# Kernel tuning notes

Measured on AMD Instinct MI355X. Metric: run time of the kernel, lower is better.

Reference implementation:

```python
import math
import jax, jax.numpy as jnp
import numpy as np

N_HEADS = 12
D_EMBED = 768
BATCH = 2
SEQ = 2048


def setup_inputs() -> dict:
    key = jax.random.key(0)
    ks = jax.random.split(key, 5)
    scale = 0.02
    return {
        "x": jax.random.normal(ks[0], (BATCH, SEQ, D_EMBED), dtype=jnp.float32),
        "w_in": jax.random.normal(ks[1], (D_EMBED, 3 * D_EMBED), dtype=jnp.float32) * scale,
        "b_in": jax.random.normal(ks[2], (3 * D_EMBED,), dtype=jnp.float32) * scale,
        "w_out": jax.random.normal(ks[3], (D_EMBED, D_EMBED), dtype=jnp.float32) * scale,
        "b_out": jax.random.normal(ks[4], (D_EMBED,), dtype=jnp.float32) * scale,
    }


def reference(x, w_in, b_in, w_out, b_out):
    # x: [B, S, D]
    B, S, D = x.shape
    H = N_HEADS
    dh = D // H
    # Fused QKV projection: [B, S, 3D]
    qkv = x @ w_in + b_in
    q, k, v = jnp.split(qkv, 3, axis=-1)
    # [B, S, D] -> [B, H, S, dh]
    def to_heads(t):
        return t.reshape(B, S, H, dh).transpose(0, 2, 1, 3)
    q, k, v = to_heads(q), to_heads(k), to_heads(v)
    # Scaled dot-product attention (non-causal, masked=False default)
    scale = 1.0 / math.sqrt(dh)
    scores = jnp.einsum("bhqd,bhkd->bhqk", q, k) * scale  # [B, H, S, S]
    probs = jax.nn.softmax(scores, axis=-1)
    out = jnp.einsum("bhqk,bhkd->bhqd", probs, v)  # [B, H, S, dh]
    # Merge heads: [B, S, D]
    out = out.transpose(0, 2, 1, 3).reshape(B, S, D)
    return out @ w_out + b_out
```

## Files before the change

### kernel.cpp

```cpp
#include <hip/hip_runtime.h>
#include <stdint.h>

#define B_   2
#define S_   2048
#define D_   768
#define H_   12
#define DH_  64
#define N3_  2304
#define M_   4096

typedef __attribute__((ext_vector_type(8))) short    bf16x8;
typedef __attribute__((ext_vector_type(4))) float    f32x4;
typedef __attribute__((ext_vector_type(4))) int      i32x4;
typedef __attribute__((ext_vector_type(4))) unsigned short u16x4;
typedef _Float16 f16x4 __attribute__((ext_vector_type(4)));
typedef __fp16   h16x2 __attribute__((ext_vector_type(2)));

#define KSCALE 0.18033688011112042f

__device__ inline unsigned short f2bf(float f) {
    union { float f; unsigned u; } v; v.f = f;
    unsigned r = v.u + 0x7FFFu + ((v.u >> 16) & 1u);
    return (unsigned short)(r >> 16);
}

__device__ inline void async_copy16(const void* g, void* l) {
    __builtin_amdgcn_global_load_lds((const __attribute__((address_space(1))) void*)g,
                                     (__attribute__((address_space(3))) void*)l, 16, 0, 0);
}

__global__ __launch_bounds__(256) void prep_all(
    const float* __restrict__ x, const float* __restrict__ w_in,
    const float* __restrict__ w_out,
    unsigned short* __restrict__ xb, unsigned short* __restrict__ winT,
    unsigned short* __restrict__ woutT)
{
    __shared__ unsigned short t[32][33];
    const int gid = blockIdx.x, tid = threadIdx.x;
    if (gid < 3072) {
        int i = gid * 256 + tid;
        f32x4 v = *(const f32x4*)(x + (size_t)i * 4);
        u16x4 o;
        o.x = f2bf(v.x); o.y = f2bf(v.y); o.z = f2bf(v.z); o.w = f2bf(v.w);
        *(u16x4*)(xb + (size_t)i * 4) = o;
        return;
    }
    const float* src; unsigned short* dst; int R, C, bx, by;
    if (gid < 4800) { int b = gid - 3072; src = w_in;  dst = winT;  R = D_; C = N3_; bx = b % 72; by = b / 72; }
    else            { int b = gid - 4800; src = w_out; dst = woutT; R = D_; C = D_;  bx = b % 24; by = b / 24; }
    int c0 = bx * 32, r0 = by * 32, tx = tid & 31, ty = tid >> 5;
#pragma unroll
    for (int j = 0; j < 4; j++)
        t[ty + j * 8][tx] = f2bf(src[(size_t)(r0 + ty + j * 8) * C + c0 + tx]);
    __syncthreads();
#pragma unroll
    for (int j = 0; j < 4; j++)
        dst[(size_t)(c0 + ty + j * 8) * R + r0 + tx] = t[tx][ty + j * 8];
}

__global__ __launch_bounds__(256) void gemm_qkv(
    const unsigned short* __restrict__ A,
    const unsigned short* __restrict__ Bt,
    const float* __restrict__ bias,
    unsigned short* __restrict__ QK,
    unsigned short* __restrict__ Vt)
{
    __shared__ __align__(16) short Al[128 * 32];
    __shared__ __align__(16) short Bl[96 * 32];

    const int tid  = threadIdx.x;
    const int w    = tid >> 6;
    const int lane = tid & 63;
    const int r    = lane & 15;
    const int quad = lane >> 4;
    const int m0   = blockIdx.y * 128;
    const int n0   = blockIdx.x * 96;
    const int wm   = (w & 1) * 64;
    const int wn   = (w >> 1) * 48;
    const int K    = D_;

    f32x4 acc[4][3];
#pragma unroll
    for (int i = 0; i < 4; i++)
#pragma unroll
        for (int j = 0; j < 3; j++) acc[i][j] = f32x4{0.f, 0.f, 0.f, 0.f};

    const int c0 = tid, c1 = tid + 256;
    const size_t ga0 = (size_t)(m0 + (c0 >> 2)) * K + (c0 & 3) * 8;
    const size_t ga1 = (size_t)(m0 + (c1 >> 2)) * K + (c1 & 3) * 8;
    const size_t gb0 = (size_t)(n0 + (c0 >> 2)) * K + (c0 & 3) * 8;
    const size_t gb1 = (size_t)(n0 + (c1 >> 2)) * K + (c1 & 3) * 8;
    short* lA0 = &Al[(0 * 256 + w * 64) * 8];
    short* lA1 = &Al[(1 * 256 + w * 64) * 8];
    short* lB0 = &Bl[(0 * 256 + w * 64) * 8];
    short* lB1 = &Bl[(1 * 256 + w * 64) * 8];

    for (int k0 = 0; k0 < K; k0 += 32) {
        __syncthreads();
        async_copy16(A  + ga0 + k0, lA0);
        async_copy16(A  + ga1 + k0, lA1);
        async_copy16(Bt + gb0 + k0, lB0);
        if (w < 2) async_copy16(Bt + gb1 + k0, lB1);
        __syncthreads();

        bf16x8 af[4], bf[3];
#pragma unroll
        for (int mi = 0; mi < 4; mi++)
            af[mi] = *(const bf16x8*)&Al[(wm + mi * 16 + r) * 32 + quad * 8];
#pragma unroll
        for (int ni = 0; ni < 3; ni++)
            bf[ni] = *(const bf16x8*)&Bl[(wn + ni * 16 + r) * 32 + quad * 8];
#pragma unroll
        for (int mi = 0; mi < 4; mi++)
#pragma unroll
            for (int ni = 0; ni < 3; ni++)
                acc[mi][ni] = __builtin_amdgcn_mfma_f32_16x16x32_bf16(
                    af[mi], bf[ni], acc[mi][ni], 0, 0, 0);
    }

    const size_t one = (size_t)B_ * H_ * S_ * DH_;
#pragma unroll
    for (int ni = 0; ni < 3; ni++) {
        int col  = n0 + wn + ni * 16 + r;
        float bv = bias[col];
        int part = col / 768;
        int cc   = col - part * 768;
        int h    = cc >> 6;
        int d    = cc & 63;
        if (part == 2) {
#pragma unroll
            for (int mi = 0; mi < 4; mi++) {
                int row0 = m0 + wm + mi * 16 + quad * 4;
                int b    = row0 >> 11;
                int s0   = row0 & 2047;
                u16x4 pk;
#pragma unroll
                for (int i = 0; i < 4; i++) {
                    union { _Float16 h; unsigned short s; } cv;
                    cv.h = (_Float16)(acc[mi][ni][i] + bv);
                    pk[i] = cv.s;
                }
                *(u16x4*)&Vt[(((size_t)(b * H_ + h)) * DH_ + d) * S_ + s0] = pk;
            }
        } else {
            float scl = (part == 1) ? KSCALE : 1.0f;
            unsigned short* dst = QK + (size_t)part * one;
#pragma unroll
            for (int mi = 0; mi < 4; mi++) {
#pragma unroll
                for (int i = 0; i < 4; i++) {
                    int row = m0 + wm + mi * 16 + quad * 4 + i;
                    int b   = row >> 11;
                    int s   = row & 2047;
                    dst[(((size_t)(b * H_ + h)) * S_ + s) * DH_ + d] =
                        f2bf((acc[mi][ni][i] + bv) * scl);
                }
            }
        }
    }
}

__global__ __launch_bounds__(256) void gemm_out(
    const unsigned short* __restrict__ A,
    const unsigned short* __restrict__ Bt,
    const float* __restrict__ bias,
    float* __restrict__ Cf)
{
    __shared__ __align__(16) short Al[64 * 32];
    __shared__ __align__(16) short Bl[64 * 32];

    const int tid  = threadIdx.x;
    const int w    = tid >> 6;
    const int lane = tid & 63;
    const int r    = lane & 15;
    const int quad = lane >> 4;
    const int m0   = blockIdx.y * 64;
    const int n0   = blockIdx.x * 64;
    const int wm   = (w & 1) * 32;
    const int wn   = (w >> 1) * 32;
    const int K    = D_;
    const int N    = D_;

    f32x4 acc[2][2];
#pragma unroll
    for (int i = 0; i < 2; i++)
#pragma unroll
        for (int j = 0; j < 2; j++) acc[i][j] = f32x4{0.f, 0.f, 0.f, 0.f};

    const size_t ga = (size_t)(m0 + (tid >> 2)) * K + (tid & 3) * 8;
    const size_t gb = (size_t)(n0 + (tid >> 2)) * K + (tid & 3) * 8;
    short* lA = &Al[(w * 64) * 8];
    short* lB = &Bl[(w * 64) * 8];

    for (int k0 = 0; k0 < K; k0 += 32) {
        __syncthreads();
        async_copy16(A  + ga + k0, lA);
        async_copy16(Bt + gb + k0, lB);
        __syncthreads();

        bf16x8 af[2], bf[2];
#pragma unroll
        for (int mi = 0; mi < 2; mi++)
            af[mi] = *(const bf16x8*)&Al[(wm + mi * 16 + r) * 32 + quad * 8];
#pragma unroll
        for (int ni = 0; ni < 2; ni++)
            bf[ni] = *(const bf16x8*)&Bl[(wn + ni * 16 + r) * 32 + quad * 8];
#pragma unroll
        for (int mi = 0; mi < 2; mi++)
#pragma unroll
            for (int ni = 0; ni < 2; ni++)
                acc[mi][ni] = __builtin_amdgcn_mfma_f32_16x16x32_bf16(
                    af[mi], bf[ni], acc[mi][ni], 0, 0, 0);
    }

#pragma unroll
    for (int ni = 0; ni < 2; ni++) {
        int col  = n0 + wn + ni * 16 + r;
        float bv = bias[col];
#pragma unroll
        for (int mi = 0; mi < 2; mi++) {
#pragma unroll
            for (int i = 0; i < 4; i++) {
                int row = m0 + wm + mi * 16 + quad * 4 + i;
                Cf[(size_t)row * N + col] = acc[mi][ni][i] + bv;
            }
        }
    }
}

__global__ __launch_bounds__(256) void attn_kernel(
    const unsigned short* __restrict__ Q,
    const unsigned short* __restrict__ K,
    const unsigned short* __restrict__ Vt,
    unsigned short* __restrict__ On0,
    unsigned short* __restrict__ On1,
    float* __restrict__ lbuf)
{
    __shared__ __align__(16) short Kl[64 * 64];
    __shared__ __align__(16) short Vl[64 * 64];

    const int tid  = threadIdx.x;
    const int w    = tid >> 6;
    const int lane = tid & 63;
    const int r    = lane & 15;
    const int quad = lane >> 4;
    const int xk   = r & 7;
    const int bid  = blockIdx.x;
    const int bh   = bid % 24;
    const int t2   = bid / 24;
    const int qb   = t2 & 15;
    const int half = t2 >> 4;
    const size_t baseQK = (size_t)bh * S_ * DH_;
    const size_t baseV  = (size_t)bh * DH_ * S_;
    const int q0   = qb * 128;
    const int kt0  = half * 16;

    bf16x8 qf[2][2];
#pragma unroll
    for (int qt = 0; qt < 2; qt++) {
        const unsigned short* qp =
            Q + baseQK + (size_t)(q0 + w * 32 + qt * 16 + r) * DH_ + quad * 8;
        qf[qt][0] = *(const bf16x8*)(qp);
        qf[qt][1] = *(const bf16x8*)(qp + 32);
    }

    f32x4 o[2][4];
    f32x4 lacc[2];
#pragma unroll
    for (int qt = 0; qt < 2; qt++) {
        lacc[qt] = f32x4{0.f, 0.f, 0.f, 0.f};
#pragma unroll
        for (int nb = 0; nb < 4; nb++) o[qt][nb] = f32x4{0.f, 0.f, 0.f, 0.f};
    }

    const f16x4 ONES = {(_Float16)1.f, (_Float16)1.f, (_Float16)1.f, (_Float16)1.f};

    const int srw = tid >> 3, schk = tid & 7;
    const unsigned short* kg = K  + baseQK + (size_t)kt0 * 4096 + tid * 8;
    const unsigned short* vg = Vt + baseV + (size_t)kt0 * 64 + (size_t)srw * S_ + schk * 8;
    const int lb = srw * 64 + (schk ^ (srw & 7)) * 8;

    i32x4 kreg[2], vreg[2];
    kreg[0] = *(const i32x4*)(kg);
    kreg[1] = *(const i32x4*)(kg + 2048);
    vreg[0] = *(const i32x4*)(vg);
    vreg[1] = *(const i32x4*)(vg + 32 * S_);

    for (int it = 0; it < 16; it++) {
        __syncthreads();
        *(i32x4*)&Kl[lb]        = kreg[0];
        *(i32x4*)&Kl[lb + 2048] = kreg[1];
        *(i32x4*)&Vl[lb]        = vreg[0];
        *(i32x4*)&Vl[lb + 2048] = vreg[1];
        __syncthreads();

        if (it != 15) {
            const unsigned short* kn = kg + (it + 1) * 4096;
            const unsigned short* vn = vg + (it + 1) * 64;
            kreg[0] = *(const i32x4*)(kn);
            kreg[1] = *(const i32x4*)(kn + 2048);
            vreg[0] = *(const i32x4*)(vn);
            vreg[1] = *(const i32x4*)(vn + 32 * S_);
        }

        f32x4 sa[2][4];
#pragma unroll
        for (int qt = 0; qt < 2; qt++)
#pragma unroll
            for (int kb = 0; kb < 4; kb++) sa[qt][kb] = f32x4{0.f, 0.f, 0.f, 0.f};
#pragma unroll
        for (int t = 0; t < 2; t++)
#pragma unroll
            for (int kb = 0; kb < 4; kb++) {
                bf16x8 kf = *(const bf16x8*)&Kl[(kb * 16 + r) * 64 + ((t * 4 + quad) ^ xk) * 8];
#pragma unroll
                for (int qt = 0; qt < 2; qt++)
                    sa[qt][kb] = __builtin_amdgcn_mfma_f32_16x16x32_bf16(
                        kf, qf[qt][t], sa[qt][kb], 0, 0, 0);
            }

        f16x4 pf[2][4];
#pragma unroll
        for (int qt = 0; qt < 2; qt++)
#pragma unroll
            for (int kb = 0; kb < 4; kb++) {
                float p0 = __builtin_amdgcn_exp2f(sa[qt][kb][0]);
                float p1 = __builtin_amdgcn_exp2f(sa[qt][kb][1]);
                float p2 = __builtin_amdgcn_exp2f(sa[qt][kb][2]);
                float p3 = __builtin_amdgcn_exp2f(sa[qt][kb][3]);
                union { f16x4 v; h16x2 h[2]; } u;
                u.h[0] = __builtin_amdgcn_cvt_pkrtz(p0, p1);
                u.h[1] = __builtin_amdgcn_cvt_pkrtz(p2, p3);
                pf[qt][kb] = u.v;
            }

#pragma unroll
        for (int kb = 0; kb < 4; kb++) {
#pragma unroll
            for (int nb = 0; nb < 4; nb++) {
                f16x4 vf = *(const f16x4*)&Vl[(nb * 16 + r) * 64 +
                                              ((kb * 2 + (quad >> 1)) ^ xk) * 8 + (quad & 1) * 4];
#pragma unroll
                for (int qt = 0; qt < 2; qt++)
                    o[qt][nb] = __builtin_amdgcn_mfma_f32_16x16x16f16(
                        pf[qt][kb], vf, o[qt][nb], 0, 0, 0);
            }
#pragma unroll
            for (int qt = 0; qt < 2; qt++)
                lacc[qt] = __builtin_amdgcn_mfma_f32_16x16x16f16(
                    pf[qt][kb], ONES, lacc[qt], 0, 0, 0);
        }
    }

    unsigned short* Ob = half ? On1 : On0;
#pragma unroll
    for (int qt = 0; qt < 2; qt++)
#pragma unroll
        for (int i = 0; i < 4; i++) {
            int s = q0 + w * 32 + qt * 16 + quad * 4 + i;
            size_t row = (size_t)bh * S_ + s;
            if (r == 0) lbuf[half * (24 * S_) + row] = lacc[qt][i];
#pragma unroll
            for (int nb = 0; nb < 4; nb++) {
                union { _Float16 h; unsigned short u; } cv;
                cv.h = (_Float16)o[qt][nb][i];
                Ob[row * 64 + nb * 16 + r] = cv.u;
            }
        }
}

__global__ void combine_attn(const unsigned short* __restrict__ On0,
                             const unsigned short* __restrict__ On1,
                             const float* __restrict__ lbuf,
                             unsigned short* __restrict__ Out)
{
    int g   = blockIdx.x * 256 + threadIdx.x;
    int hd8 = g % 96;
    int bs  = g / 96;
    int h   = hd8 >> 3;
    int d8  = (hd8 & 7) * 8;
    size_t row = ((size_t)((bs >> 11) * H_ + h)) * S_ + (bs & 2047);
    float inv = 1.0f / (lbuf[row] + lbuf[24 * S_ + row]);
    i32x4 a = *(const i32x4*)&On0[row * 64 + d8];
    i32x4 c = *(const i32x4*)&On1[row * 64 + d8];
    const _Float16* fa = (const _Float16*)&a;
    const _Float16* fc = (const _Float16*)&c;
    unsigned short tmp[8];
#pragma unroll
    for (int j = 0; j < 8; j++)
        tmp[j] = f2bf(((float)fa[j] + (float)fc[j]) * inv);
    *(i32x4*)&Out[(size_t)bs * D_ + h * 64 + d8] = *(const i32x4*)tmp;
}

extern "C" void kernel_launch(void* const* d_in, const int* in_sizes, int n_in,
                              void* d_out, int out_size, void* d_ws, size_t ws_size,
                              hipStream_t stream) {
    const float* x     = (const float*)d_in[0];
    const float* w_in  = (const float*)d_in[1];
    const float* b_in  = (const float*)d_in[2];
    const float* w_out = (const float*)d_in[3];
    const float* b_out = (const float*)d_in[4];
    float* out = (float*)d_out;
    char* ws = (char*)d_ws;

    unsigned short* xb    = (unsigned short*)(ws);
    unsigned short* winT  = (unsigned short*)(ws + 6291456);
    unsigned short* woutT = (unsigned short*)(ws + 9830400);
    unsigned short* QKV   = (unsigned short*)(ws + 11010048);
    unsigned short* On1   = (unsigned short*)(ws + 29884416);

    const size_t one = (size_t)B_ * H_ * S_ * DH_;
    unsigned short* Vtbuf = QKV + 2 * one;
    unsigned short* On0   = xb;
    float*          lbuf  = (float*)winT;
    unsigned short* attnO = QKV;

    prep_all<<<5376, 256, 0, stream>>>(x, w_in, w_out, xb, winT, woutT);

    gemm_qkv<<<dim3(N3_ / 96, M_ / 128), 256, 0, stream>>>(
        xb, winT, b_in, QKV, Vtbuf);

    attn_kernel<<<24 * 16 * 2, 256, 0, stream>>>(
        QKV, QKV + one, Vtbuf, On0, On1, lbuf);

    combine_attn<<<1536, 256, 0, stream>>>(On0, On1, lbuf, attnO);

    gemm_out<<<dim3(D_ / 64, M_ / 64), 256, 0, stream>>>(
        attnO, woutT, b_out, out);
}
```

Before: 158.9 us.

## Split attention keys four ways and fuse partial combine into output GEMM

The attention kernel now splits the key range into four chunks instead of two, doubling the grid to 1536 blocks. Each chunk writes unnormalised fp16 partial outputs and row sums. The separate combine kernel is removed, and the output projection GEMM now loads the four partials, sums and normalises them, converts to bf16 and writes the A tile to LDS itself. This removes one launch and a round trip through memory, but it makes the GEMM's A load synchronous and four times larger per k-step and recomputes the normalisation for every column block.

Result: slower. 180.2 us (+13.4%).

```diff
diff --git a/kernel.cpp b/kernel.cpp
--- a/kernel.cpp
+++ b/kernel.cpp
@@ -17,6 +17,8 @@
 typedef __fp16   h16x2 __attribute__((ext_vector_type(2)));
 
 #define KSCALE 0.18033688011112042f
+#define LSTRIDE (24 * S_)
+#define ONE_EL  ((size_t)24 * S_ * DH_)
 
 __device__ inline unsigned short f2bf(float f) {
     union { float f; unsigned u; } v; v.f = f;
@@ -161,7 +163,8 @@
 }
 
 __global__ __launch_bounds__(256) void gemm_out(
-    const unsigned short* __restrict__ A,
+    const unsigned short* __restrict__ On,
+    const float* __restrict__ lbuf,
     const unsigned short* __restrict__ Bt,
     const float* __restrict__ bias,
     float* __restrict__ Cf)
@@ -187,16 +190,41 @@
 #pragma unroll
         for (int j = 0; j < 2; j++) acc[i][j] = f32x4{0.f, 0.f, 0.f, 0.f};
 
-    const size_t ga = (size_t)(m0 + (tid >> 2)) * K + (tid & 3) * 8;
+    const int arow = tid >> 2, d8 = (tid & 3) * 8;
+    const int m = m0 + arow, bb = m >> 11, s = m & 2047;
     const size_t gb = (size_t)(n0 + (tid >> 2)) * K + (tid & 3) * 8;
-    short* lA = &Al[(w * 64) * 8];
     short* lB = &Bl[(w * 64) * 8];
 
+    i32x4 a0, a1, a2, a3; float inv;
+    auto pre = [&](int k0) {
+        int h = k0 >> 6;
+        size_t row = (size_t)(bb * H_ + h) * S_ + s;
+        size_t ob  = row * 64 + (k0 & 63) + d8;
+        a0 = *(const i32x4*)&On[ob];
+        a1 = *(const i32x4*)&On[ob + ONE_EL];
+        a2 = *(const i32x4*)&On[ob + 2 * ONE_EL];
+        a3 = *(const i32x4*)&On[ob + 3 * ONE_EL];
+        inv = 1.0f / (lbuf[row] + lbuf[LSTRIDE + row] +
+                      lbuf[2 * LSTRIDE + row] + lbuf[3 * LSTRIDE + row]);
+    };
+    pre(0);
+
     for (int k0 = 0; k0 < K; k0 += 32) {
         __syncthreads();
-        async_copy16(A  + ga + k0, lA);
+        {
+            const _Float16* p0 = (const _Float16*)&a0;
+            const _Float16* p1 = (const _Float16*)&a1;
+            const _Float16* p2 = (const _Float16*)&a2;
+            const _Float16* p3 = (const _Float16*)&a3;
+            unsigned short t8[8];
+#pragma unroll
+            for (int j = 0; j < 8; j++)
+                t8[j] = f2bf(((float)p0[j] + (float)p1[j] + (float)p2[j] + (float)p3[j]) * inv);
+            *(i32x4*)&Al[tid * 8] = *(const i32x4*)t8;
+        }
         async_copy16(Bt + gb + k0, lB);
         __syncthreads();
+        if (k0 + 32 < K) pre(k0 + 32);
 
         bf16x8 af[2], bf[2];
 #pragma unroll
@@ -232,8 +260,7 @@
     const unsigned short* __restrict__ Q,
     const unsigned short* __restrict__ K,
     const unsigned short* __restrict__ Vt,
-    unsigned short* __restrict__ On0,
-    unsigned short* __restrict__ On1,
+    unsigned short* __restrict__ On,
     float* __restrict__ lbuf)
 {
     __shared__ __align__(16) short Kl[64 * 64];
@@ -249,11 +276,11 @@
     const int bh   = bid % 24;
     const int t2   = bid / 24;
     const int qb   = t2 & 15;
-    const int half = t2 >> 4;
+    const int quarter = t2 >> 4;
     const size_t baseQK = (size_t)bh * S_ * DH_;
     const size_t baseV  = (size_t)bh * DH_ * S_;
     const int q0   = qb * 128;
-    const int kt0  = half * 16;
+    const int kt0  = quarter * 8;
 
     bf16x8 qf[2][2];
 #pragma unroll
@@ -286,7 +313,7 @@
     vreg[0] = *(const i32x4*)(vg);
     vreg[1] = *(const i32x4*)(vg + 32 * S_);
 
-    for (int it = 0; it < 16; it++) {
+    for (int it = 0; it < 8; it++) {
         __syncthreads();
         *(i32x4*)&Kl[lb]        = kreg[0];
         *(i32x4*)&Kl[lb + 2048] = kreg[1];
@@ -294,7 +321,7 @@
         *(i32x4*)&Vl[lb + 2048] = vreg[1];
         __syncthreads();
 
-        if (it != 15) {
+        if (it != 7) {
             const unsigned short* kn = kg + (it + 1) * 4096;
             const unsigned short* vn = vg + (it + 1) * 64;
             kreg[0] = *(const i32x4*)(kn);
@@ -352,14 +379,14 @@
         }
     }
 
-    unsigned short* Ob = half ? On1 : On0;
+    unsigned short* Ob = On + (size_t)quarter * ONE_EL;
 #pragma unroll
     for (int qt = 0; qt < 2; qt++)
 #pragma unroll
         for (int i = 0; i < 4; i++) {
             int s = q0 + w * 32 + qt * 16 + quad * 4 + i;
             size_t row = (size_t)bh * S_ + s;
-            if (r == 0) lbuf[half * (24 * S_) + row] = lacc[qt][i];
+            if (r == 0) lbuf[quarter * LSTRIDE + row] = lacc[qt][i];
 #pragma unroll
             for (int nb = 0; nb < 4; nb++) {
                 union { _Float16 h; unsigned short u; } cv;
@@ -367,29 +394,6 @@
                 Ob[row * 64 + nb * 16 + r] = cv.u;
             }
         }
-}
-
-__global__ void combine_attn(const unsigned short* __restrict__ On0,
-                             const unsigned short* __restrict__ On1,
-                             const float* __restrict__ lbuf,
-                             unsigned short* __restrict__ Out)
-{
-    int g   = blockIdx.x * 256 + threadIdx.x;
-    int hd8 = g % 96;
-    int bs  = g / 96;
-    int h   = hd8 >> 3;
-    int d8  = (hd8 & 7) * 8;
-    size_t row = ((size_t)((bs >> 11) * H_ + h)) * S_ + (bs & 2047);
-    float inv = 1.0f / (lbuf[row] + lbuf[24 * S_ + row]);
-    i32x4 a = *(const i32x4*)&On0[row * 64 + d8];
-    i32x4 c = *(const i32x4*)&On1[row * 64 + d8];
-    const _Float16* fa = (const _Float16*)&a;
-    const _Float16* fc = (const _Float16*)&c;
-    unsigned short tmp[8];
-#pragma unroll
-    for (int j = 0; j < 8; j++)
-        tmp[j] = f2bf(((float)fa[j] + (float)fc[j]) * inv);
-    *(i32x4*)&Out[(size_t)bs * D_ + h * 64 + d8] = *(const i32x4*)tmp;
 }
 
 extern "C" void kernel_launch(void* const* d_in, const int* in_sizes, int n_in,
@@ -407,24 +411,20 @@
     unsigned short* winT  = (unsigned short*)(ws + 6291456);
     unsigned short* woutT = (unsigned short*)(ws + 9830400);
     unsigned short* QKV   = (unsigned short*)(ws + 11010048);
-    unsigned short* On1   = (unsigned short*)(ws + 29884416);
+    unsigned short* On    = (unsigned short*)(ws + 36175872);
 
     const size_t one = (size_t)B_ * H_ * S_ * DH_;
     unsigned short* Vtbuf = QKV + 2 * one;
-    unsigned short* On0   = xb;
     float*          lbuf  = (float*)winT;
-    unsigned short* attnO = QKV;
 
     prep_all<<<5376, 256, 0, stream>>>(x, w_in, w_out, xb, winT, woutT);
 
     gemm_qkv<<<dim3(N3_ / 96, M_ / 128), 256, 0, stream>>>(
         xb, winT, b_in, QKV, Vtbuf);
 
-    attn_kernel<<<24 * 16 * 2, 256, 0, stream>>>(
-        QKV, QKV + one, Vtbuf, On0, On1, lbuf);
-
-    combine_attn<<<1536, 256, 0, stream>>>(On0, On1, lbuf, attnO);
+    attn_kernel<<<24 * 16 * 4, 256, 0, stream>>>(
+        QKV, QKV + one, Vtbuf, On, lbuf);
 
     gemm_out<<<dim3(D_ / 64, M_ / 64), 256, 0, stream>>>(
-        attnO, woutT, b_out, out);
-}
+        On, lbuf, woutT, b_out, out);
+}
```
